# Optimization experiments

Measured on AMD Instinct MI355X. Metric: run time of the kernel, lower is better.

Reference implementation:

```python
import jax, jax.numpy as jnp
import numpy as np

B, S, HID, H = 4, 2048, 1024, 16
D = HID // H  # head_dim = 64


def setup_inputs() -> dict:
    key = jax.random.key(0)
    ks = jax.random.split(key, 12)
    std = 0.02
    inp = {
        "q": jax.random.normal(ks[0], (B, S, HID), jnp.float32),
        "k": jax.random.normal(ks[1], (B, S, HID), jnp.float32),
        "v": jax.random.normal(ks[2], (B, S, HID), jnp.float32),
        # causal mask: True where attention is NOT allowed (masked_fill semantics)
        "attn_mask": jnp.broadcast_to(
            ~jnp.tril(jnp.ones((S, S), jnp.bool_)), (B, S, S)
        ),
        "Wq": jax.random.normal(ks[3], (HID, HID), jnp.float32) * std,
        "bq": jnp.zeros((HID,), jnp.float32),
        "Wk": jax.random.normal(ks[4], (HID, HID), jnp.float32) * std,
        "bk": jnp.zeros((HID,), jnp.float32),
        "Wv": jax.random.normal(ks[5], (HID, HID), jnp.float32) * std,
        "bv": jnp.zeros((HID,), jnp.float32),
        "Wo": jax.random.normal(ks[6], (HID, HID), jnp.float32) * std,
        "bo": jnp.zeros((HID,), jnp.float32),
    }
    return inp


def _split_heads(x):
    # [B, S, HID] -> [B, H, S, D]
    b, s, _ = x.shape
    return x.reshape(b, s, H, D).transpose(0, 2, 1, 3)


def reference(q, k, v, attn_mask, Wq, bq, Wk, bk, Wv, bv, Wo, bo):
    qh = _split_heads(q @ Wq.T + bq)  # [B,H,S,D]
    kh = _split_heads(k @ Wk.T + bk)
    vh = _split_heads(v @ Wv.T + bv)
    scale = 1.0 / jnp.sqrt(jnp.asarray(D, qh.dtype))
    scores = jnp.einsum("bhqd,bhkd->bhqk", qh, kh) * scale  # [B,H,S,S]
    neg = jnp.asarray(-1e9, scores.dtype)
    scores = jnp.where(attn_mask[:, None, :, :], neg, scores)
    attn = jax.nn.softmax(scores, axis=-1)
    ctx = jnp.einsum("bhqk,bhkd->bhqd", attn, vh)  # [B,H,S,D]
    ctx = ctx.transpose(0, 2, 1, 3).reshape(q.shape[0], q.shape[1], HID)
    return ctx @ Wo.T + bo
```

## Files before the change

### kernel.cpp

```cpp
#include <hip/hip_runtime.h>

typedef __attribute__((ext_vector_type(8))) short short8;
typedef __attribute__((ext_vector_type(4))) float f32x4;
typedef __attribute__((ext_vector_type(16))) float f32x16;

#define S_LEN 2048
#define HIDN  1024
#define NHEAD 16
#define DHEAD 64

__device__ __forceinline__ short f2bf(float x) {
    unsigned u = __float_as_uint(x);
    u += 0x7fffu + ((u >> 16) & 1u);
    return (short)(u >> 16);
}

typedef const __attribute__((address_space(1))) void* gas_ptr;
typedef __attribute__((address_space(3))) void* las_ptr;

__device__ __forceinline__ void gload_lds16(const void* g, void* l) {
    __builtin_amdgcn_global_load_lds((gas_ptr)g, (las_ptr)l, 16, 0, 0);
}

__device__ __forceinline__ unsigned cvtpk(float lo, float hi_) {
    unsigned r;
    asm("v_cvt_pk_bf16_f32 %0, %1, %2" : "=v"(r) : "v"(lo), "v"(hi_));
    return r;
}

__device__ __forceinline__ void plswap(unsigned& x, unsigned& y) {
    asm("v_permlane32_swap_b32 %0, %1" : "+&v"(x), "+&v"(y));
}

__device__ __forceinline__ short8 mk8(unsigned a, unsigned b, unsigned c, unsigned d) {
    union { unsigned u[4]; short8 s; } t;
    t.u[0] = a; t.u[1] = b; t.u[2] = c; t.u[3] = d;
    return t.s;
}

__global__ __launch_bounds__(256) void cvt_all(const float* __restrict__ q,
                                               const float* __restrict__ k,
                                               const float* __restrict__ v,
                                               const float* __restrict__ Wq,
                                               const float* __restrict__ Wk,
                                               const float* __restrict__ Wv,
                                               const float* __restrict__ Wo,
                                               short* __restrict__ qb,
                                               short* __restrict__ kb,
                                               short* __restrict__ vb,
                                               short* __restrict__ wqb,
                                               short* __restrict__ wkb,
                                               short* __restrict__ wvb,
                                               short* __restrict__ wob) {
    int bid = blockIdx.x;
    const float* in;
    short* out;
    int base;
    if (bid < 2048) {
        int wsel = bid >> 9;
        base = bid & 511;
        in  = wsel == 0 ? Wq  : wsel == 1 ? Wk  : wsel == 2 ? Wv  : Wo;
        out = wsel == 0 ? wqb : wsel == 1 ? wkb : wsel == 2 ? wvb : wob;
    } else if (bid < 6144)  { in = q; out = qb; base = bid - 2048; }
    else if (bid < 10240)   { in = k; out = kb; base = bid - 6144; }
    else                    { in = v; out = vb; base = bid - 10240; }
    int i = (base * 256 + threadIdx.x) * 8;
    float4 a = *(const float4*)(in + i);
    float4 b = *(const float4*)(in + i + 4);
    short8 o;
    o[0] = f2bf(a.x); o[1] = f2bf(a.y); o[2] = f2bf(a.z); o[3] = f2bf(a.w);
    o[4] = f2bf(b.x); o[5] = f2bf(b.y); o[6] = f2bf(b.z); o[7] = f2bf(b.w);
    *(short8*)(out + i) = o;
}

__device__ __forceinline__ void gemm_k64_db(const short* A, const short* Wb,
                                            short* As0, short* As1,
                                            short* Bs0, short* Bs1,
                                            f32x4 acc[4][4], int m0, int n0) {
    int tid = threadIdx.x;
    int w = tid >> 6, l = tid & 63, g = l >> 4, r = l & 15;
    int wm = w >> 1, wn = w & 1;
    int r7 = r & 7;

    int rowin = l >> 3;
    int scol = ((l & 7) ^ rowin) * 8;
    int dst = l * 8;

#pragma unroll
    for (int i = 0; i < 4; i++) {
        int c = w * 4 + i;
        int row = c * 8 + rowin;
        gload_lds16(A + (size_t)(m0 + row) * HIDN + scol, As0 + c * 512 + dst);
        gload_lds16(Wb + (size_t)(n0 + row) * HIDN + scol, Bs0 + c * 512 + dst);
    }
    __syncthreads();

    for (int kt = 0; kt < HIDN / 64; ++kt) {
        short* Asc = (kt & 1) ? As1 : As0;
        short* Bsc = (kt & 1) ? Bs1 : Bs0;
        short* Asn = (kt & 1) ? As0 : As1;
        short* Bsn = (kt & 1) ? Bs0 : Bs1;
        if (kt + 1 < HIDN / 64) {
            int kc = (kt + 1) * 64;
#pragma unroll
            for (int i = 0; i < 4; i++) {
                int c = w * 4 + i;
                int row = c * 8 + rowin;
                gload_lds16(A + (size_t)(m0 + row) * HIDN + kc + scol, Asn + c * 512 + dst);
                gload_lds16(Wb + (size_t)(n0 + row) * HIDN + kc + scol, Bsn + c * 512 + dst);
            }
        }
        short8 af[4][2], bfr[4][2];
#pragma unroll
        for (int i = 0; i < 4; i++)
#pragma unroll
            for (int ks = 0; ks < 2; ks++)
                af[i][ks] = *(const short8*)(Asc + (wm * 64 + i * 16 + r) * 64 +
                                             ((((ks << 2) + g) ^ r7) << 3));
#pragma unroll
        for (int j = 0; j < 4; j++)
#pragma unroll
            for (int ks = 0; ks < 2; ks++)
                bfr[j][ks] = *(const short8*)(Bsc + (wn * 64 + j * 16 + r) * 64 +
                                              ((((ks << 2) + g) ^ r7) << 3));
        __builtin_amdgcn_s_setprio(1);
#pragma unroll
        for (int i = 0; i < 4; i++)
#pragma unroll
            for (int j = 0; j < 4; j++) {
                acc[i][j] = __builtin_amdgcn_mfma_f32_16x16x32_bf16(af[i][0], bfr[j][0], acc[i][j], 0, 0, 0);
                acc[i][j] = __builtin_amdgcn_mfma_f32_16x16x32_bf16(af[i][1], bfr[j][1], acc[i][j], 0, 0, 0);
            }
        __builtin_amdgcn_s_setprio(0);
        __syncthreads();
    }
}

__global__ __launch_bounds__(256) void gemm_qkv(const short* __restrict__ qb,
                                                const short* __restrict__ kb,
                                                const short* __restrict__ vb,
                                                const short* __restrict__ Wqb,
                                                const short* __restrict__ Wkb,
                                                const short* __restrict__ Wvb,
                                                const float* __restrict__ bq,
                                                const float* __restrict__ bk,
                                                const float* __restrict__ bv,
                                                short* __restrict__ Qh,
                                                short* __restrict__ Kh,
                                                short* __restrict__ VhT,
                                                float qscale) {
    int which = blockIdx.x >> 9;
    int bid = blockIdx.x & 511;
    const short* A = which == 0 ? qb : which == 1 ? kb : vb;
    const short* Wb = which == 0 ? Wqb : which == 1 ? Wkb : Wvb;
    const float* bias = which == 0 ? bq : which == 1 ? bk : bv;
    short* Out = which == 0 ? Qh : which == 1 ? Kh : VhT;
    float oscale = which == 0 ? qscale : 1.0f;
    int omode = which == 2 ? 1 : 0;

    int mt = bid & 63, nt = bid >> 6;
    int m0 = mt * 128, n0 = nt * 128;
    int tid = threadIdx.x;
    int w = tid >> 6, l = tid & 63, g = l >> 4, r = l & 15;
    int wm = w >> 1, wn = w & 1;

    __shared__ short As0[128 * 64], As1[128 * 64];
    __shared__ short Bs0[128 * 64], Bs1[128 * 64];

    f32x4 acc[4][4];
#pragma unroll
    for (int i = 0; i < 4; i++)
#pragma unroll
        for (int j = 0; j < 4; j++) acc[i][j] = (f32x4){0.f, 0.f, 0.f, 0.f};

    gemm_k64_db(A, Wb, As0, As1, Bs0, Bs1, acc, m0, n0);

#pragma unroll
    for (int j = 0; j < 4; j++) {
        int n_g = n0 + wn * 64 + j * 16 + r;
        float bv2 = bias[n_g];
        int h = n_g >> 6, d = n_g & 63;
#pragma unroll
        for (int i = 0; i < 4; i++) {
#pragma unroll
            for (int rr = 0; rr < 4; rr++) {
                int m_g = m0 + wm * 64 + i * 16 + g * 4 + rr;
                float val = (acc[i][j][rr] + bv2) * oscale;
                int b = m_g >> 11, s = m_g & 2047;
                size_t idx = (omode == 0)
                    ? (((size_t)(b * NHEAD + h)) * S_LEN + s) * DHEAD + d
                    : (((size_t)(b * NHEAD + h)) * DHEAD + d) * S_LEN + s;
                Out[idx] = f2bf(val);
            }
        }
    }
}

__global__ __launch_bounds__(256) void gemm_out(const short* __restrict__ A,
                                                const short* __restrict__ Wb,
                                                const float* __restrict__ bias,
                                                float* __restrict__ Out) {
    int mt = blockIdx.x & 63, nt = blockIdx.x >> 6;
    int m0 = mt * 128, n0 = nt * 128;
    int tid = threadIdx.x;
    int w = tid >> 6, l = tid & 63, g = l >> 4, r = l & 15;
    int wm = w >> 1, wn = w & 1;

    __shared__ short As0[128 * 64], As1[128 * 64];
    __shared__ short Bs0[128 * 64], Bs1[128 * 64];

    f32x4 acc[4][4];
#pragma unroll
    for (int i = 0; i < 4; i++)
#pragma unroll
        for (int j = 0; j < 4; j++) acc[i][j] = (f32x4){0.f, 0.f, 0.f, 0.f};

    gemm_k64_db(A, Wb, As0, As1, Bs0, Bs1, acc, m0, n0);

#pragma unroll
    for (int j = 0; j < 4; j++) {
        int n_g = n0 + wn * 64 + j * 16 + r;
        float bv = bias[n_g];
#pragma unroll
        for (int i = 0; i < 4; i++) {
#pragma unroll
            for (int rr = 0; rr < 4; rr++) {
                int m_g = m0 + wm * 64 + i * 16 + g * 4 + rr;
                Out[(size_t)m_g * HIDN + n_g] = acc[i][j][rr] + bv;
            }
        }
    }
}

__global__ __launch_bounds__(256) void attn_kernel(const short* __restrict__ Qh,
                                                   const short* __restrict__ Kh,
                                                   const short* __restrict__ VhT,
                                                   short* __restrict__ ctx) {
    int bid = blockIdx.x;
    int j = bid >> 6;
    int bh = ((bid >> 3) & 7) * 8 + (bid & 7);
    int tid = threadIdx.x;
    int w = tid >> 6, l = tid & 63;
    int ql = l & 31, hi = l >> 5;

    __shared__ short KV[2][2][64 * 64];

    const short* Qb = Qh + (size_t)bh * (S_LEN * DHEAD);
    const short* Kb = Kh + (size_t)bh * (S_LEN * DHEAD);
    const short* Vb = VhT + (size_t)bh * (DHEAD * S_LEN);

    int srow0 = tid >> 3, srow1 = srow0 + 32;
    int scol = (tid & 7) * 8;
    int wo0 = srow0 * 64 + (scol ^ ((srow0 & 7) << 3));
    int wo1 = srow1 * 64 + (scol ^ ((srow1 & 7) << 3));

    int r0 = ql, r1 = 32 + ql;
    int sw = (ql & 7) << 3;
    int ch = hi * 8;

    int b = bh >> 4, h = bh & 15;

    for (int half = 0; half < 2; ++half) {
        int qt = half ? (15 - j) : j;
        int q_g = qt * 128 + w * 32 + ql;
        const short* qp = Qb + (size_t)q_g * DHEAD + hi * 8;
        short8 qf0 = *(const short8*)(qp);
        short8 qf1 = *(const short8*)(qp + 16);
        short8 qf2 = *(const short8*)(qp + 32);
        short8 qf3 = *(const short8*)(qp + 48);

        f32x16 accA, accB;
#pragma unroll
        for (int i = 0; i < 16; ++i) { accA[i] = 0.f; accB[i] = 0.f; }
        float lrun = 0.f;

        int ktp = (qt * 128 + w * 32) >> 6;
        int nt = 2 * qt + 2;

        __syncthreads();
        {
            short8 k0 = *(const short8*)(Kb + srow0 * 64 + scol);
            short8 k1 = *(const short8*)(Kb + srow1 * 64 + scol);
            short8 v0 = *(const short8*)(Vb + (size_t)srow0 * S_LEN + scol);
            short8 v1 = *(const short8*)(Vb + (size_t)srow1 * S_LEN + scol);
            *(short8*)(&KV[0][0][wo0]) = k0;
            *(short8*)(&KV[0][0][wo1]) = k1;
            *(short8*)(&KV[0][1][wo0]) = v0;
            *(short8*)(&KV[0][1][wo1]) = v1;
        }

        for (int kt = 0; kt < nt; ++kt) {
            __syncthreads();
            int cur = kt & 1;
            short8 pk0, pk1, pv0, pv1;
            bool pf = (kt + 1 < nt);
            if (pf) {
                const short* Kt = Kb + (kt + 1) * (64 * DHEAD);
                const short* Vt = Vb + (kt + 1) * 64;
                pk0 = *(const short8*)(Kt + srow0 * 64 + scol);
                pk1 = *(const short8*)(Kt + srow1 * 64 + scol);
                pv0 = *(const short8*)(Vt + (size_t)srow0 * S_LEN + scol);
                pv1 = *(const short8*)(Vt + (size_t)srow1 * S_LEN + scol);
            }
            if (kt <= ktp) {
                const short* Ksb = &KV[cur][0][0];
                const short* Vsb = &KV[cur][1][0];
                f32x16 st0, st1;
#pragma unroll
                for (int i = 0; i < 16; ++i) { st0[i] = 0.f; st1[i] = 0.f; }
                {
                    short8 kA, kB;
                    kA = *(const short8*)(Ksb + r0 * 64 + ((0 + ch) ^ sw));
                    kB = *(const short8*)(Ksb + r1 * 64 + ((0 + ch) ^ sw));
                    __builtin_amdgcn_s_setprio(1);
                    st0 = __builtin_amdgcn_mfma_f32_32x32x16_bf16(kA, qf0, st0, 0, 0, 0);
                    st1 = __builtin_amdgcn_mfma_f32_32x32x16_bf16(kB, qf0, st1, 0, 0, 0);
                    __builtin_amdgcn_s_setprio(0);
                    kA = *(const short8*)(Ksb + r0 * 64 + ((16 + ch) ^ sw));
                    kB = *(const short8*)(Ksb + r1 * 64 + ((16 + ch) ^ sw));
                    __builtin_amdgcn_s_setprio(1);
                    st0 = __builtin_amdgcn_mfma_f32_32x32x16_bf16(kA, qf1, st0, 0, 0, 0);
                    st1 = __builtin_amdgcn_mfma_f32_32x32x16_bf16(kB, qf1, st1, 0, 0, 0);
                    __builtin_amdgcn_s_setprio(0);
                    kA = *(const short8*)(Ksb + r0 * 64 + ((32 + ch) ^ sw));
                    kB = *(const short8*)(Ksb + r1 * 64 + ((32 + ch) ^ sw));
                    __builtin_amdgcn_s_setprio(1);
                    st0 = __builtin_amdgcn_mfma_f32_32x32x16_bf16(kA, qf2, st0, 0, 0, 0);
                    st1 = __builtin_amdgcn_mfma_f32_32x32x16_bf16(kB, qf2, st1, 0, 0, 0);
                    __builtin_amdgcn_s_setprio(0);
                    kA = *(const short8*)(Ksb + r0 * 64 + ((48 + ch) ^ sw));
                    kB = *(const short8*)(Ksb + r1 * 64 + ((48 + ch) ^ sw));
                    __builtin_amdgcn_s_setprio(1);
                    st0 = __builtin_amdgcn_mfma_f32_32x32x16_bf16(kA, qf3, st0, 0, 0, 0);
                    st1 = __builtin_amdgcn_mfma_f32_32x32x16_bf16(kB, qf3, st1, 0, 0, 0);
                    __builtin_amdgcn_s_setprio(0);
                }
                float p[32];
#pragma unroll
                for (int i = 0; i < 16; ++i) { p[i] = st0[i]; p[16 + i] = st1[i]; }
                if (kt == ktp) {
#pragma unroll
                    for (int i = 0; i < 32; ++i) {
                        int kl = (i & 3) + 8 * ((i >> 2) & 3) + 32 * (i >> 4) + 4 * hi;
                        if (kt * 64 + kl > q_g) p[i] = -1e30f;
                    }
                }
#pragma unroll
                for (int i = 0; i < 32; ++i) p[i] = exp2f(p[i]);
                float t[16];
#pragma unroll
                for (int i = 0; i < 16; ++i) t[i] = p[i] + p[i + 16];
#pragma unroll
                for (int i = 0; i < 8; ++i) t[i] = t[i] + t[i + 8];
#pragma unroll
                for (int i = 0; i < 4; ++i) t[i] = t[i] + t[i + 4];
                float rs = (t[0] + t[1]) + (t[2] + t[3]);
                rs += __shfl_xor(rs, 32);
                lrun += rs;
                {
                    unsigned u0 = cvtpk(p[0], p[1]);
                    unsigned u1 = cvtpk(p[2], p[3]);
                    unsigned u2 = cvtpk(p[4], p[5]);
                    unsigned u3 = cvtpk(p[6], p[7]);
                    plswap(u0, u2);
                    plswap(u1, u3);
                    short8 pfA = mk8(u0, u1, u2, u3);
                    unsigned u4 = cvtpk(p[8], p[9]);
                    unsigned u5 = cvtpk(p[10], p[11]);
                    unsigned u6 = cvtpk(p[12], p[13]);
                    unsigned u7 = cvtpk(p[14], p[15]);
                    plswap(u4, u6);
                    plswap(u5, u7);
                    short8 pfB = mk8(u4, u5, u6, u7);
                    short8 vA0 = *(const short8*)(Vsb + r0 * 64 + ((0 + ch) ^ sw));
                    short8 vB0 = *(const short8*)(Vsb + r1 * 64 + ((0 + ch) ^ sw));
                    short8 vA1 = *(const short8*)(Vsb + r0 * 64 + ((16 + ch) ^ sw));
                    short8 vB1 = *(const short8*)(Vsb + r1 * 64 + ((16 + ch) ^ sw));
                    __builtin_amdgcn_s_setprio(1);
                    accA = __builtin_amdgcn_mfma_f32_32x32x16_bf16(vA0, pfA, accA, 0, 0, 0);
                    accB = __builtin_amdgcn_mfma_f32_32x32x16_bf16(vB0, pfA, accB, 0, 0, 0);
                    accA = __builtin_amdgcn_mfma_f32_32x32x16_bf16(vA1, pfB, accA, 0, 0, 0);
                    accB = __builtin_amdgcn_mfma_f32_32x32x16_bf16(vB1, pfB, accB, 0, 0, 0);
                    __builtin_amdgcn_s_setprio(0);
                }
                {
                    unsigned u0 = cvtpk(p[16], p[17]);
                    unsigned u1 = cvtpk(p[18], p[19]);
                    unsigned u2 = cvtpk(p[20], p[21]);
                    unsigned u3 = cvtpk(p[22], p[23]);
                    plswap(u0, u2);
                    plswap(u1, u3);
                    short8 pfC = mk8(u0, u1, u2, u3);
                    unsigned u4 = cvtpk(p[24], p[25]);
                    unsigned u5 = cvtpk(p[26], p[27]);
                    unsigned u6 = cvtpk(p[28], p[29]);
                    unsigned u7 = cvtpk(p[30], p[31]);
                    plswap(u4, u6);
                    plswap(u5, u7);
                    short8 pfD = mk8(u4, u5, u6, u7);
                    short8 vA2 = *(const short8*)(Vsb + r0 * 64 + ((32 + ch) ^ sw));
                    short8 vB2 = *(const short8*)(Vsb + r1 * 64 + ((32 + ch) ^ sw));
                    short8 vA3 = *(const short8*)(Vsb + r0 * 64 + ((48 + ch) ^ sw));
                    short8 vB3 = *(const short8*)(Vsb + r1 * 64 + ((48 + ch) ^ sw));
                    __builtin_amdgcn_s_setprio(1);
                    accA = __builtin_amdgcn_mfma_f32_32x32x16_bf16(vA2, pfC, accA, 0, 0, 0);
                    accB = __builtin_amdgcn_mfma_f32_32x32x16_bf16(vB2, pfC, accB, 0, 0, 0);
                    accA = __builtin_amdgcn_mfma_f32_32x32x16_bf16(vA3, pfD, accA, 0, 0, 0);
                    accB = __builtin_amdgcn_mfma_f32_32x32x16_bf16(vB3, pfD, accB, 0, 0, 0);
                    __builtin_amdgcn_s_setprio(0);
                }
            }
            if (pf) {
                int nb = (kt + 1) & 1;
                *(short8*)(&KV[nb][0][wo0]) = pk0;
                *(short8*)(&KV[nb][0][wo1]) = pk1;
                *(short8*)(&KV[nb][1][wo0]) = pv0;
                *(short8*)(&KV[nb][1][wo1]) = pv1;
            }
        }

        float inv = 1.0f / lrun;
        short* cb = ctx + ((size_t)(b * S_LEN + q_g)) * HIDN + h * DHEAD;
#pragma unroll
        for (int i = 0; i < 16; ++i) {
            int d0 = (i & 3) + 8 * (i >> 2) + 4 * hi;
            cb[d0] = f2bf(accA[i] * inv);
            cb[32 + d0] = f2bf(accB[i] * inv);
        }
    }
}

extern "C" void kernel_launch(void* const* d_in, const int* in_sizes, int n_in,
                              void* d_out, int out_size, void* d_ws, size_t ws_size,
                              hipStream_t stream) {
    const float* q  = (const float*)d_in[0];
    const float* k  = (const float*)d_in[1];
    const float* v  = (const float*)d_in[2];
    const float* Wq = (const float*)d_in[4];
    const float* bq = (const float*)d_in[5];
    const float* Wk = (const float*)d_in[6];
    const float* bk = (const float*)d_in[7];
    const float* Wv = (const float*)d_in[8];
    const float* bv = (const float*)d_in[9];
    const float* Wo = (const float*)d_in[10];
    const float* bo = (const float*)d_in[11];

    char* ws = (char*)d_ws;
    const size_t ACT = (size_t)8192 * 1024 * 2;
    const size_t WSZ = (size_t)1024 * 1024 * 2;
    short* Qh  = (short*)(ws);
    short* Kh  = (short*)(ws + ACT);
    short* VhT = (short*)(ws + 2 * ACT);
    short* qb  = (short*)(ws + 3 * ACT);
    short* kb  = (short*)(ws + 4 * ACT);
    short* vb  = (short*)(ws + 5 * ACT);
    short* ctx = qb;
    short* Wqb = (short*)(ws + 6 * ACT);
    short* Wkb = (short*)(ws + 6 * ACT + WSZ);
    short* Wvb = (short*)(ws + 6 * ACT + 2 * WSZ);
    short* Wob = (short*)(ws + 6 * ACT + 3 * WSZ);

    cvt_all<<<14336, 256, 0, stream>>>(q, k, v, Wq, Wk, Wv, Wo,
                                       qb, kb, vb, Wqb, Wkb, Wvb, Wob);

    const float QSCALE = 0.125f * 1.44269504088896340736f;
    gemm_qkv<<<1536, 256, 0, stream>>>(qb, kb, vb, Wqb, Wkb, Wvb, bq, bk, bv,
                                       Qh, Kh, VhT, QSCALE);

    attn_kernel<<<512, 256, 0, stream>>>(Qh, Kh, VhT, ctx);

    gemm_out<<<512, 256, 0, stream>>>(ctx, Wob, bo, (float*)d_out);
}
```

Measured before the change: 199.5 us.

## Process paired causal query tiles concurrently in 512-thread attention blocks sharing K/V

The attention kernel now runs both query tiles of a causal pair (j and 15-j) at the same time in one 512-thread block, with eight warps split into two groups, instead of processing them one after the other. Each K/V tile is loaded into shared memory once and used by both groups, which halves the K/V staging traffic per tile and doubles the warps available to hide latency. Grid indexing is remapped so that block pairs cover mirrored tile indices. The cost is that the warps of the short tile sit idle through the barriers of the longer loop, and the larger block can lower occupancy.

```diff
diff --git a/kernel.cpp b/kernel.cpp
--- a/kernel.cpp
+++ b/kernel.cpp
@@ -232,16 +232,22 @@
     }
 }
 
-__global__ __launch_bounds__(256) void attn_kernel(const short* __restrict__ Qh,
+__global__ __launch_bounds__(512) void attn_kernel(const short* __restrict__ Qh,
                                                    const short* __restrict__ Kh,
                                                    const short* __restrict__ VhT,
                                                    short* __restrict__ ctx) {
     int bid = blockIdx.x;
-    int j = bid >> 6;
-    int bh = ((bid >> 3) & 7) * 8 + (bid & 7);
+    int m = bid >> 8;
+    int u = bid & 255;
+    int q2 = u >> 6;
+    int bh = ((u >> 3) & 7) * 8 + (u & 7);
+    int j = m ? (7 - q2) : q2;
+    int qtB = 15 - j;
     int tid = threadIdx.x;
     int w = tid >> 6, l = tid & 63;
     int ql = l & 31, hi = l >> 5;
+    int wq = w & 3, grp = w >> 2;
+    int qt = grp ? qtB : j;
 
     __shared__ short KV[2][2][64 * 64];
 
@@ -249,184 +255,168 @@
     const short* Kb = Kh + (size_t)bh * (S_LEN * DHEAD);
     const short* Vb = VhT + (size_t)bh * (DHEAD * S_LEN);
 
-    int srow0 = tid >> 3, srow1 = srow0 + 32;
+    int srow = tid >> 3;
     int scol = (tid & 7) * 8;
-    int wo0 = srow0 * 64 + (scol ^ ((srow0 & 7) << 3));
-    int wo1 = srow1 * 64 + (scol ^ ((srow1 & 7) << 3));
+    int wo = srow * 64 + (scol ^ ((srow & 7) << 3));
 
     int r0 = ql, r1 = 32 + ql;
     int sw = (ql & 7) << 3;
     int ch = hi * 8;
-
     int b = bh >> 4, h = bh & 15;
 
-    for (int half = 0; half < 2; ++half) {
-        int qt = half ? (15 - j) : j;
-        int q_g = qt * 128 + w * 32 + ql;
-        const short* qp = Qb + (size_t)q_g * DHEAD + hi * 8;
-        short8 qf0 = *(const short8*)(qp);
-        short8 qf1 = *(const short8*)(qp + 16);
-        short8 qf2 = *(const short8*)(qp + 32);
-        short8 qf3 = *(const short8*)(qp + 48);
-
-        f32x16 accA, accB;
-#pragma unroll
-        for (int i = 0; i < 16; ++i) { accA[i] = 0.f; accB[i] = 0.f; }
-        float lrun = 0.f;
-
-        int ktp = (qt * 128 + w * 32) >> 6;
-        int nt = 2 * qt + 2;
-
+    int q_g = qt * 128 + wq * 32 + ql;
+    const short* qp = Qb + (size_t)q_g * DHEAD + hi * 8;
+    short8 qf0 = *(const short8*)(qp);
+    short8 qf1 = *(const short8*)(qp + 16);
+    short8 qf2 = *(const short8*)(qp + 32);
+    short8 qf3 = *(const short8*)(qp + 48);
+
+    f32x16 accA, accB;
+#pragma unroll
+    for (int i = 0; i < 16; ++i) { accA[i] = 0.f; accB[i] = 0.f; }
+    float lrun = 0.f;
+
+    int ktp = (qt * 128 + wq * 32) >> 6;
+    int nt = 2 * qtB + 2;
+
+    {
+        short8 k0 = *(const short8*)(Kb + srow * 64 + scol);
+        short8 v0 = *(const short8*)(Vb + (size_t)srow * S_LEN + scol);
+        *(short8*)(&KV[0][0][wo]) = k0;
+        *(short8*)(&KV[0][1][wo]) = v0;
+    }
+
+    for (int kt = 0; kt < nt; ++kt) {
         __syncthreads();
-        {
-            short8 k0 = *(const short8*)(Kb + srow0 * 64 + scol);
-            short8 k1 = *(const short8*)(Kb + srow1 * 64 + scol);
-            short8 v0 = *(const short8*)(Vb + (size_t)srow0 * S_LEN + scol);
-            short8 v1 = *(const short8*)(Vb + (size_t)srow1 * S_LEN + scol);
-            *(short8*)(&KV[0][0][wo0]) = k0;
-            *(short8*)(&KV[0][0][wo1]) = k1;
-            *(short8*)(&KV[0][1][wo0]) = v0;
-            *(short8*)(&KV[0][1][wo1]) = v1;
-        }
-
-        for (int kt = 0; kt < nt; ++kt) {
-            __syncthreads();
-            int cur = kt & 1;
-            short8 pk0, pk1, pv0, pv1;
-            bool pf = (kt + 1 < nt);
-            if (pf) {
-                const short* Kt = Kb + (kt + 1) * (64 * DHEAD);
-                const short* Vt = Vb + (kt + 1) * 64;
-                pk0 = *(const short8*)(Kt + srow0 * 64 + scol);
-                pk1 = *(const short8*)(Kt + srow1 * 64 + scol);
-                pv0 = *(const short8*)(Vt + (size_t)srow0 * S_LEN + scol);
-                pv1 = *(const short8*)(Vt + (size_t)srow1 * S_LEN + scol);
-            }
-            if (kt <= ktp) {
-                const short* Ksb = &KV[cur][0][0];
-                const short* Vsb = &KV[cur][1][0];
-                f32x16 st0, st1;
-#pragma unroll
-                for (int i = 0; i < 16; ++i) { st0[i] = 0.f; st1[i] = 0.f; }
-                {
-                    short8 kA, kB;
-                    kA = *(const short8*)(Ksb + r0 * 64 + ((0 + ch) ^ sw));
-                    kB = *(const short8*)(Ksb + r1 * 64 + ((0 + ch) ^ sw));
-                    __builtin_amdgcn_s_setprio(1);
-                    st0 = __builtin_amdgcn_mfma_f32_32x32x16_bf16(kA, qf0, st0, 0, 0, 0);
-                    st1 = __builtin_amdgcn_mfma_f32_32x32x16_bf16(kB, qf0, st1, 0, 0, 0);
-                    __builtin_amdgcn_s_setprio(0);
-                    kA = *(const short8*)(Ksb + r0 * 64 + ((16 + ch) ^ sw));
-                    kB = *(const short8*)(Ksb + r1 * 64 + ((16 + ch) ^ sw));
-                    __builtin_amdgcn_s_setprio(1);
-                    st0 = __builtin_amdgcn_mfma_f32_32x32x16_bf16(kA, qf1, st0, 0, 0, 0);
-                    st1 = __builtin_amdgcn_mfma_f32_32x32x16_bf16(kB, qf1, st1, 0, 0, 0);
-                    __builtin_amdgcn_s_setprio(0);
-                    kA = *(const short8*)(Ksb + r0 * 64 + ((32 + ch) ^ sw));
-                    kB = *(const short8*)(Ksb + r1 * 64 + ((32 + ch) ^ sw));
-                    __builtin_amdgcn_s_setprio(1);
-                    st0 = __builtin_amdgcn_mfma_f32_32x32x16_bf16(kA, qf2, st0, 0, 0, 0);
-                    st1 = __builtin_amdgcn_mfma_f32_32x32x16_bf16(kB, qf2, st1, 0, 0, 0);
-                    __builtin_amdgcn_s_setprio(0);
-                    kA = *(const short8*)(Ksb + r0 * 64 + ((48 + ch) ^ sw));
-                    kB = *(const short8*)(Ksb + r1 * 64 + ((48 + ch) ^ sw));
-                    __builtin_amdgcn_s_setprio(1);
-                    st0 = __builtin_amdgcn_mfma_f32_32x32x16_bf16(kA, qf3, st0, 0, 0, 0);
-                    st1 = __builtin_amdgcn_mfma_f32_32x32x16_bf16(kB, qf3, st1, 0, 0, 0);
-                    __builtin_amdgcn_s_setprio(0);
+        int cur = kt & 1;
+        short8 pk0, pv0;
+        bool pf = (kt + 1 < nt);
+        if (pf) {
+            pk0 = *(const short8*)(Kb + (kt + 1) * (64 * DHEAD) + srow * 64 + scol);
+            pv0 = *(const short8*)(Vb + (size_t)srow * S_LEN + (kt + 1) * 64 + scol);
+        }
+        if (kt <= ktp) {
+            const short* Ksb = &KV[cur][0][0];
+            const short* Vsb = &KV[cur][1][0];
+            f32x16 st0, st1;
+#pragma unroll
+            for (int i = 0; i < 16; ++i) { st0[i] = 0.f; st1[i] = 0.f; }
+            {
+                short8 kA, kB;
+                kA = *(const short8*)(Ksb + r0 * 64 + ((0 + ch) ^ sw));
+                kB = *(const short8*)(Ksb + r1 * 64 + ((0 + ch) ^ sw));
+                __builtin_amdgcn_s_setprio(1);
+                st0 = __builtin_amdgcn_mfma_f32_32x32x16_bf16(kA, qf0, st0, 0, 0, 0);
+                st1 = __builtin_amdgcn_mfma_f32_32x32x16_bf16(kB, qf0, st1, 0, 0, 0);
+                __builtin_amdgcn_s_setprio(0);
+                kA = *(const short8*)(Ksb + r0 * 64 + ((16 + ch) ^ sw));
+                kB = *(const short8*)(Ksb + r1 * 64 + ((16 + ch) ^ sw));
+                __builtin_amdgcn_s_setprio(1);
+                st0 = __builtin_amdgcn_mfma_f32_32x32x16_bf16(kA, qf1, st0, 0, 0, 0);
+                st1 = __builtin_amdgcn_mfma_f32_32x32x16_bf16(kB, qf1, st1, 0, 0, 0);
+                __builtin_amdgcn_s_setprio(0);
+                kA = *(const short8*)(Ksb + r0 * 64 + ((32 + ch) ^ sw));
+                kB = *(const short8*)(Ksb + r1 * 64 + ((32 + ch) ^ sw));
+                __builtin_amdgcn_s_setprio(1);
+                st0 = __builtin_amdgcn_mfma_f32_32x32x16_bf16(kA, qf2, st0, 0, 0, 0);
+                st1 = __builtin_amdgcn_mfma_f32_32x32x16_bf16(kB, qf2, st1, 0, 0, 0);
+                __builtin_amdgcn_s_setprio(0);
+                kA = *(const short8*)(Ksb + r0 * 64 + ((48 + ch) ^ sw));
+                kB = *(const short8*)(Ksb + r1 * 64 + ((48 + ch) ^ sw));
+                __builtin_amdgcn_s_setprio(1);
+                st0 = __builtin_amdgcn_mfma_f32_32x32x16_bf16(kA, qf3, st0, 0, 0, 0);
+                st1 = __builtin_amdgcn_mfma_f32_32x32x16_bf16(kB, qf3, st1, 0, 0, 0);
+                __builtin_amdgcn_s_setprio(0);
+            }
+            float p[32];
+#pragma unroll
+            for (int i = 0; i < 16; ++i) { p[i] = st0[i]; p[16 + i] = st1[i]; }
+            if (kt == ktp) {
+#pragma unroll
+                for (int i = 0; i < 32; ++i) {
+                    int kl = (i & 3) + 8 * ((i >> 2) & 3) + 32 * (i >> 4) + 4 * hi;
+                    if (kt * 64 + kl > q_g) p[i] = -1e30f;
                 }
-                float p[32];
-#pragma unroll
-                for (int i = 0; i < 16; ++i) { p[i] = st0[i]; p[16 + i] = st1[i]; }
-                if (kt == ktp) {
-#pragma unroll
-                    for (int i = 0; i < 32; ++i) {
-                        int kl = (i & 3) + 8 * ((i >> 2) & 3) + 32 * (i >> 4) + 4 * hi;
-                        if (kt * 64 + kl > q_g) p[i] = -1e30f;
-                    }
-                }
-#pragma unroll
-                for (int i = 0; i < 32; ++i) p[i] = exp2f(p[i]);
-                float t[16];
-#pragma unroll
-                for (int i = 0; i < 16; ++i) t[i] = p[i] + p[i + 16];
-#pragma unroll
-                for (int i = 0; i < 8; ++i) t[i] = t[i] + t[i + 8];
-#pragma unroll
-                for (int i = 0; i < 4; ++i) t[i] = t[i] + t[i + 4];
-                float rs = (t[0] + t[1]) + (t[2] + t[3]);
-                rs += __shfl_xor(rs, 32);
-                lrun += rs;
-                {
-                    unsigned u0 = cvtpk(p[0], p[1]);
-                    unsigned u1 = cvtpk(p[2], p[3]);
-                    unsigned u2 = cvtpk(p[4], p[5]);
-                    unsigned u3 = cvtpk(p[6], p[7]);
-                    plswap(u0, u2);
-                    plswap(u1, u3);
-                    short8 pfA = mk8(u0, u1, u2, u3);
-                    unsigned u4 = cvtpk(p[8], p[9]);
-                    unsigned u5 = cvtpk(p[10], p[11]);
-                    unsigned u6 = cvtpk(p[12], p[13]);
-                    unsigned u7 = cvtpk(p[14], p[15]);
-                    plswap(u4, u6);
-                    plswap(u5, u7);
-                    short8 pfB = mk8(u4, u5, u6, u7);
-                    short8 vA0 = *(const short8*)(Vsb + r0 * 64 + ((0 + ch) ^ sw));
-                    short8 vB0 = *(const short8*)(Vsb + r1 * 64 + ((0 + ch) ^ sw));
-                    short8 vA1 = *(const short8*)(Vsb + r0 * 64 + ((16 + ch) ^ sw));
-                    short8 vB1 = *(const short8*)(Vsb + r1 * 64 + ((16 + ch) ^ sw));
-                    __builtin_amdgcn_s_setprio(1);
-                    accA = __builtin_amdgcn_mfma_f32_32x32x16_bf16(vA0, pfA, accA, 0, 0, 0);
-                    accB = __builtin_amdgcn_mfma_f32_32x32x16_bf16(vB0, pfA, accB, 0, 0, 0);
-                    accA = __builtin_amdgcn_mfma_f32_32x32x16_bf16(vA1, pfB, accA, 0, 0, 0);
-                    accB = __builtin_amdgcn_mfma_f32_32x32x16_bf16(vB1, pfB, accB, 0, 0, 0);
-                    __builtin_amdgcn_s_setprio(0);
-                }
-                {
-                    unsigned u0 = cvtpk(p[16], p[17]);
-                    unsigned u1 = cvtpk(p[18], p[19]);
-                    unsigned u2 = cvtpk(p[20], p[21]);
-                    unsigned u3 = cvtpk(p[22], p[23]);
-                    plswap(u0, u2);
-                    plswap(u1, u3);
-                    short8 pfC = mk8(u0, u1, u2, u3);
-                    unsigned u4 = cvtpk(p[24], p[25]);
-                    unsigned u5 = cvtpk(p[26], p[27]);
-                    unsigned u6 = cvtpk(p[28], p[29]);
-                    unsigned u7 = cvtpk(p[30], p[31]);
-                    plswap(u4, u6);
-                    plswap(u5, u7);
-                    short8 pfD = mk8(u4, u5, u6, u7);
-                    short8 vA2 = *(const short8*)(Vsb + r0 * 64 + ((32 + ch) ^ sw));
-                    short8 vB2 = *(const short8*)(Vsb + r1 * 64 + ((32 + ch) ^ sw));
-                    short8 vA3 = *(const short8*)(Vsb + r0 * 64 + ((48 + ch) ^ sw));
-                    short8 vB3 = *(const short8*)(Vsb + r1 * 64 + ((48 + ch) ^ sw));
-                    __builtin_amdgcn_s_setprio(1);
-                    accA = __builtin_amdgcn_mfma_f32_32x32x16_bf16(vA2, pfC, accA, 0, 0, 0);
-                    accB = __builtin_amdgcn_mfma_f32_32x32x16_bf16(vB2, pfC, accB, 0, 0, 0);
-                    accA = __builtin_amdgcn_mfma_f32_32x32x16_bf16(vA3, pfD, accA, 0, 0, 0);
-                    accB = __builtin_amdgcn_mfma_f32_32x32x16_bf16(vB3, pfD, accB, 0, 0, 0);
-                    __builtin_amdgcn_s_setprio(0);
-                }
-            }
-            if (pf) {
-                int nb = (kt + 1) & 1;
-                *(short8*)(&KV[nb][0][wo0]) = pk0;
-                *(short8*)(&KV[nb][0][wo1]) = pk1;
-                *(short8*)(&KV[nb][1][wo0]) = pv0;
-                *(short8*)(&KV[nb][1][wo1]) = pv1;
-            }
-        }
-
-        float inv = 1.0f / lrun;
-        short* cb = ctx + ((size_t)(b * S_LEN + q_g)) * HIDN + h * DHEAD;
-#pragma unroll
-        for (int i = 0; i < 16; ++i) {
-            int d0 = (i & 3) + 8 * (i >> 2) + 4 * hi;
-            cb[d0] = f2bf(accA[i] * inv);
-            cb[32 + d0] = f2bf(accB[i] * inv);
-        }
+            }
+#pragma unroll
+            for (int i = 0; i < 32; ++i) p[i] = exp2f(p[i]);
+            float t[16];
+#pragma unroll
+            for (int i = 0; i < 16; ++i) t[i] = p[i] + p[i + 16];
+#pragma unroll
+            for (int i = 0; i < 8; ++i) t[i] = t[i] + t[i + 8];
+#pragma unroll
+            for (int i = 0; i < 4; ++i) t[i] = t[i] + t[i + 4];
+            float rs = (t[0] + t[1]) + (t[2] + t[3]);
+            rs += __shfl_xor(rs, 32);
+            lrun += rs;
+            {
+                unsigned u0 = cvtpk(p[0], p[1]);
+                unsigned u1 = cvtpk(p[2], p[3]);
+                unsigned u2 = cvtpk(p[4], p[5]);
+                unsigned u3 = cvtpk(p[6], p[7]);
+                plswap(u0, u2);
+                plswap(u1, u3);
+                short8 pfA = mk8(u0, u1, u2, u3);
+                unsigned u4 = cvtpk(p[8], p[9]);
+                unsigned u5 = cvtpk(p[10], p[11]);
+                unsigned u6 = cvtpk(p[12], p[13]);
+                unsigned u7 = cvtpk(p[14], p[15]);
+                plswap(u4, u6);
+                plswap(u5, u7);
+                short8 pfB = mk8(u4, u5, u6, u7);
+                short8 vA0 = *(const short8*)(Vsb + r0 * 64 + ((0 + ch) ^ sw));
+                short8 vB0 = *(const short8*)(Vsb + r1 * 64 + ((0 + ch) ^ sw));
+                short8 vA1 = *(const short8*)(Vsb + r0 * 64 + ((16 + ch) ^ sw));
+                short8 vB1 = *(const short8*)(Vsb + r1 * 64 + ((16 + ch) ^ sw));
+                __builtin_amdgcn_s_setprio(1);
+                accA = __builtin_amdgcn_mfma_f32_32x32x16_bf16(vA0, pfA, accA, 0, 0, 0);
+                accB = __builtin_amdgcn_mfma_f32_32x32x16_bf16(vB0, pfA, accB, 0, 0, 0);
+                accA = __builtin_amdgcn_mfma_f32_32x32x16_bf16(vA1, pfB, accA, 0, 0, 0);
+                accB = __builtin_amdgcn_mfma_f32_32x32x16_bf16(vB1, pfB, accB, 0, 0, 0);
+                __builtin_amdgcn_s_setprio(0);
+            }
+            {
+                unsigned u0 = cvtpk(p[16], p[17]);
+                unsigned u1 = cvtpk(p[18], p[19]);
+                unsigned u2 = cvtpk(p[20], p[21]);
+                unsigned u3 = cvtpk(p[22], p[23]);
+                plswap(u0, u2);
+                plswap(u1, u3);
+                short8 pfC = mk8(u0, u1, u2, u3);
+                unsigned u4 = cvtpk(p[24], p[25]);
+                unsigned u5 = cvtpk(p[26], p[27]);
+                unsigned u6 = cvtpk(p[28], p[29]);
+                unsigned u7 = cvtpk(p[30], p[31]);
+                plswap(u4, u6);
+                plswap(u5, u7);
+                short8 pfD = mk8(u4, u5, u6, u7);
+                short8 vA2 = *(const short8*)(Vsb + r0 * 64 + ((32 + ch) ^ sw));
+                short8 vB2 = *(const short8*)(Vsb + r1 * 64 + ((32 + ch) ^ sw));
+                short8 vA3 = *(const short8*)(Vsb + r0 * 64 + ((48 + ch) ^ sw));
+                short8 vB3 = *(const short8*)(Vsb + r1 * 64 + ((48 + ch) ^ sw));
+                __builtin_amdgcn_s_setprio(1);
+                accA = __builtin_amdgcn_mfma_f32_32x32x16_bf16(vA2, pfC, accA, 0, 0, 0);
+                accB = __builtin_amdgcn_mfma_f32_32x32x16_bf16(vB2, pfC, accB, 0, 0, 0);
+                accA = __builtin_amdgcn_mfma_f32_32x32x16_bf16(vA3, pfD, accA, 0, 0, 0);
+                accB = __builtin_amdgcn_mfma_f32_32x32x16_bf16(vB3, pfD, accB, 0, 0, 0);
+                __builtin_amdgcn_s_setprio(0);
+            }
+        }
+        if (pf) {
+            int nb = (kt + 1) & 1;
+            *(short8*)(&KV[nb][0][wo]) = pk0;
+            *(short8*)(&KV[nb][1][wo]) = pv0;
+        }
+    }
+
+    float inv = 1.0f / lrun;
+    short* cb = ctx + ((size_t)(b * S_LEN + q_g)) * HIDN + h * DHEAD;
+#pragma unroll
+    for (int i = 0; i < 16; ++i) {
+        int d0 = (i & 3) + 8 * (i >> 2) + 4 * hi;
+        cb[d0] = f2bf(accA[i] * inv);
+        cb[32 + d0] = f2bf(accB[i] * inv);
     }
 }
 
@@ -467,7 +457,7 @@
     gemm_qkv<<<1536, 256, 0, stream>>>(qb, kb, vb, Wqb, Wkb, Wvb, bq, bk, bv,
                                        Qh, Kh, VhT, QSCALE);
 
-    attn_kernel<<<512, 256, 0, stream>>>(Qh, Kh, VhT, ctx);
+    attn_kernel<<<512, 512, 0, stream>>>(Qh, Kh, VhT, ctx);
 
     gemm_out<<<512, 256, 0, stream>>>(ctx, Wob, bo, (float*)d_out);
 }
```

Measured after the change: 183.4 us. -8.1%, faster.
